# Optimization experiments

Measured on AMD Instinct MI355X. Metric: run time of the kernel, lower is better.

Reference implementation:

```python
import jax, jax.numpy as jnp
import numpy as np
from functools import partial

VOCAB = 32000
HID = 512
B, T = 16, 256


def setup_inputs() -> dict:
    key = jax.random.key(0)
    ks = jax.random.split(key, 14)
    s = 1.0 / np.sqrt(HID)
    u = lambda k, shape: jax.random.uniform(k, shape, jnp.float32, -s, s)
    inp = {
        "input_s": jax.random.randint(ks[0], (B, T), 0, VOCAB),
        "output_s": jax.random.randint(ks[1], (B, T), 0, VOCAB),
        "emb": jax.random.normal(ks[2], (VOCAB, HID), jnp.float32),
        "Wf": u(ks[3], (HID, 2 * HID)), "bf": u(ks[4], (HID,)),
        "Wi": u(ks[5], (HID, 2 * HID)), "bi": u(ks[6], (HID,)),
        "Wc": u(ks[7], (HID, 2 * HID)), "bc": u(ks[8], (HID,)),
        "Wo": u(ks[9], (HID, 2 * HID)), "bo": u(ks[10], (HID,)),
        "fcW": u(ks[11], (VOCAB, HID)), "fcb": u(ks[12], (VOCAB,)),
    }
    return inp


def reference(input_s, output_s, emb, Wf, bf, Wi, bi, Wc, bc, Wo, bo, fcW, fcb):
    bsz, width = input_s.shape
    x = emb[input_s]                      # [B, T, H]
    xs = jnp.swapaxes(x, 0, 1)            # [T, B, H] for scan
    h0 = jnp.zeros((bsz, HID), x.dtype)
    c0 = jnp.zeros((bsz, HID), x.dtype)

    def step(carry, xt):
        h, c = carry
        z = jnp.concatenate([h, xt], axis=1)       # [B, 2H], order (h, x) as in source
        f = jax.nn.sigmoid(z @ Wf.T + bf)
        i = jax.nn.sigmoid(z @ Wi.T + bi)
        cb = jnp.tanh(z @ Wc.T + bc)
        c = c * f + i * cb
        o = z @ Wo.T + bo                           # NOTE: no sigmoid (faithful to source)
        h = o * jnp.tanh(c)
        return (h, c), h

    _, hs = jax.lax.scan(step, (h0, c0), xs)        # hs: [T, B, H]
    hs = jnp.swapaxes(hs, 0, 1)                     # [B, T, H]
    logits = jnp.einsum("bth,vh->btv", hs, fcW) + fcb   # [B, T, V]
    logp = jax.nn.log_softmax(logits, axis=-1)
    nll = -jnp.take_along_axis(logp, output_s[..., None], axis=-1)[..., 0]
    loss = jnp.mean(nll)
    return logits, loss
```

## Files before the change

kernel.cpp:

```cpp
#include <hip/hip_runtime.h>

typedef unsigned short u16;
typedef __attribute__((ext_vector_type(8))) short bf16x8;
typedef __attribute__((ext_vector_type(4))) float f32x4;
typedef __attribute__((ext_vector_type(2))) float f32x2;
typedef __attribute__((ext_vector_type(4))) unsigned u32x4;

#define T_LEN 256
#define HID   512
#define VOCABN 32000
#define SCAN_WGS 16
#define FC_WORKERS 480
#define N_TILES 8000

__device__ __forceinline__ u16 f2bf(float f) {
  union { float f; unsigned u; } v; v.f = f;
  return (u16)((v.u + 0x7fffu + ((v.u >> 16) & 1u)) >> 16);
}
__device__ __forceinline__ float fast_tanh(float x) {
  return 1.f - 2.f / (__expf(2.f * x) + 1.f);
}

typedef __attribute__((address_space(1))) void as1v;
typedef __attribute__((address_space(3))) void as3v;
__device__ __forceinline__ void gload_lds16(const u16* g, u16* l) {
  __builtin_amdgcn_global_load_lds((as1v*)g, (as3v*)l, 16, 0, 0);
}

__global__ __launch_bounds__(256) void k_gather(const int* __restrict__ idx,
                                                const float* __restrict__ emb,
                                                u16* __restrict__ X) {
  int row0 = blockIdx.x * 8;
  for (int i = threadIdx.x; i < 8 * 128; i += 256) {
    int r = i >> 7, cb = i & 127;
    int row = row0 + r;
    int e = idx[row];
    float4 v = *(const float4*)&emb[(long)e * HID + cb * 4];
    ushort4 o; o.x = f2bf(v.x); o.y = f2bf(v.y); o.z = f2bf(v.z); o.w = f2bf(v.w);
    *(ushort4*)&X[(long)row * HID + cb * 4] = o;
  }
}

__global__ __launch_bounds__(256) void k_wconv(const float* __restrict__ Wf, const float* __restrict__ Wi,
                                               const float* __restrict__ Wc, const float* __restrict__ Wo,
                                               const float* __restrict__ bfv, const float* __restrict__ biv,
                                               const float* __restrict__ bcv, const float* __restrict__ bov,
                                               u16* __restrict__ Wh, u16* __restrict__ Wx,
                                               float* __restrict__ bias4) {
  int i = blockIdx.x * 256 + threadIdx.x;
  int r = i >> 7, kb = i & 127;
  int gate = r >> 9, j = r & 511;
  const float* W = gate == 0 ? Wf : gate == 1 ? Wi : gate == 2 ? Wc : Wo;
  float4 vh = *(const float4*)&W[(long)j * 1024 + kb * 4];
  float4 vx = *(const float4*)&W[(long)j * 1024 + 512 + kb * 4];
  ushort4 oh; oh.x = f2bf(vh.x); oh.y = f2bf(vh.y); oh.z = f2bf(vh.z); oh.w = f2bf(vh.w);
  ushort4 ox; ox.x = f2bf(vx.x); ox.y = f2bf(vx.y); ox.z = f2bf(vx.z); ox.w = f2bf(vx.w);
  *(ushort4*)&Wh[(long)r * 512 + kb * 4] = oh;
  *(ushort4*)&Wx[(long)r * 512 + kb * 4] = ox;
  if (kb == 0) {
    const float* bsrc = gate == 0 ? bfv : gate == 1 ? biv : gate == 2 ? bcv : bov;
    bias4[r] = bsrc[j];
  }
}

__global__ __launch_bounds__(256) void k_fcconv(const float* __restrict__ Wsrc, u16* __restrict__ Wdst) {
  long c = (long)blockIdx.x * 256 + threadIdx.x;
  float4 v = *(const float4*)&Wsrc[c * 4];
  ushort4 o; o.x = f2bf(v.x); o.y = f2bf(v.y); o.z = f2bf(v.z); o.w = f2bf(v.w);
  *(ushort4*)&Wdst[c * 4] = o;
}

__global__ __launch_bounds__(256) void k_gemm(const u16* __restrict__ A, const u16* __restrict__ B,
                                              const float* __restrict__ bias, float* __restrict__ C,
                                              int N) {
  __shared__ __align__(16) u16 As[128 * 32];
  __shared__ __align__(16) u16 Bs[128 * 32];
  const int K = 512;
  int tid = threadIdx.x, wave = tid >> 6, lane = tid & 63;
  int nbx = gridDim.x, nby = gridDim.y;
  int id = blockIdx.y * nbx + blockIdx.x;
  int nwg = nbx * nby, q = nwg >> 3;
  int swz = (id & 7) * q + (id >> 3);
  int bm = swz % nby, bn = swz / nby;
  int wr = wave >> 1, wc = wave & 1;
  f32x4 acc[4][4] = {};
  const u16* ga = A + (long)(bm * 128 + (tid >> 2)) * K + (tid & 3) * 8;
  const u16* gb = B + (long)(bn * 128 + (tid >> 2)) * K + (tid & 3) * 8;
  u16* lA = &As[wave * 512];
  u16* lB = &Bs[wave * 512];
  for (int kk = 0; kk < K; kk += 32) {
    gload_lds16(ga + kk, lA);
    gload_lds16(ga + 64 * K + kk, lA + 2048);
    gload_lds16(gb + kk, lB);
    gload_lds16(gb + 64 * K + kk, lB + 2048);
    __syncthreads();
    bf16x8 af[4], bfr[4];
    int arow = wr * 64 + (lane & 15);
    int brow = wc * 64 + (lane & 15);
    int kcol = (lane >> 4) * 8;
#pragma unroll
    for (int m = 0; m < 4; m++) af[m] = *(const bf16x8*)&As[(arow + m * 16) * 32 + kcol];
#pragma unroll
    for (int n = 0; n < 4; n++) bfr[n] = *(const bf16x8*)&Bs[(brow + n * 16) * 32 + kcol];
#pragma unroll
    for (int m = 0; m < 4; m++)
#pragma unroll
      for (int n = 0; n < 4; n++)
        acc[m][n] = __builtin_amdgcn_mfma_f32_16x16x32_bf16(af[m], bfr[n], acc[m][n], 0, 0, 0);
    __syncthreads();
  }
  int c0 = bn * 128 + wc * 64 + (lane & 15);
  int r0 = bm * 128 + wr * 64 + (lane >> 4) * 4;
#pragma unroll
  for (int n = 0; n < 4; n++) {
    float bv = bias[c0 + n * 16];
#pragma unroll
    for (int m = 0; m < 4; m++) {
      f32x4 v = acc[m][n];
#pragma unroll
      for (int rr = 0; rr < 4; rr++)
        C[(long)(r0 + m * 16 + rr) * N + (c0 + n * 16)] = v[rr] + bv;
    }
  }
}

__global__ __launch_bounds__(256, 2) void k_fused(
    const u16* __restrict__ Wh, const float* __restrict__ xw,
    u16* __restrict__ hs, unsigned* __restrict__ vf,
    const u16* __restrict__ fcWb, const float* __restrict__ fcb,
    float* __restrict__ C, float* __restrict__ part) {
  __shared__ __align__(16) char smraw[33408];
  int tid = threadIdx.x, wave = tid >> 6, lane = tid & 63;

  if (blockIdx.x < SCAN_WGS) {
    float* gates = (float*)smraw;
    u16*   Ash   = (u16*)(smraw + 17024);
    int g = blockIdx.x;
    int l4 = lane & 15, hi = lane >> 4;
    bf16x8 wreg[2][16];
#pragma unroll
    for (int n = 0; n < 2; n++) {
      int c = wave * 32 + n * 16 + l4;
      int grow = ((c >> 5) << 9) + (g << 5) + (c & 31);
      const u16* base = Wh + ((long)grow << 9) + (hi << 3);
#pragma unroll
      for (int kt = 0; kt < 16; kt++) wreg[n][kt] = *(const bf16x8*)(base + (kt << 5));
    }
    __builtin_amdgcn_s_setprio(1);

    float cs0 = 0.f, cs1 = 0.f;
    int u0 = (tid & 15) * 2, b = tid >> 4;
    const float* xwt = xw + ((long)b << 8) * 2048 + (g << 5) + u0;
    unsigned* vfp = vf + g * 32;

    for (int t = 0; t < T_LEN; t++) {
      f32x2 xv[4];
#pragma unroll
      for (int gt = 0; gt < 4; gt++) xv[gt] = *(const f32x2*)(xwt + (long)t * 2048 + (gt << 9));

      f32x4 acc[2] = {};
      if (t > 0) {
        if (wave == 0) {
          const u16* hrow = hs + (((long)(t - 1) * 16 + l4) << 9) + (hi << 3);
          bf16x8 af[16];
          for (;;) {
#pragma unroll
            for (int kt = 0; kt < 16; kt++)
              asm volatile("global_load_dwordx4 %0, %1, off sc0 sc1"
                           : "=v"(af[kt]) : "v"(hrow + (kt << 5)) : "memory");
            asm volatile("s_waitcnt vmcnt(0)" ::: "memory");
            __builtin_amdgcn_sched_barrier(0);
            unsigned mx = 0;
#pragma unroll
            for (int kt = 0; kt < 16; kt++) {
              u32x4 d = __builtin_bit_cast(u32x4, af[kt]);
              unsigned m0 = d.x > d.y ? d.x : d.y;
              unsigned m1 = d.z > d.w ? d.z : d.w;
              unsigned m2 = m0 > m1 ? m0 : m1;
              mx = mx > m2 ? mx : m2;
            }
            if (__all(mx != 0xFFFFFFFFu)) break;
            __builtin_amdgcn_s_sleep(2);
          }
#pragma unroll
          for (int kt = 0; kt < 16; kt++)
            *(bf16x8*)&Ash[(kt << 9) + (lane << 3)] = af[kt];
          if (lane == 0) {
            unsigned tv = (unsigned)t;
            asm volatile("global_store_dword %0, %1, off sc0 sc1" :: "v"(vfp), "v"(tv) : "memory");
          }
        }
        __syncthreads();
#pragma unroll
        for (int kt = 0; kt < 16; kt++) {
          bf16x8 afr = *(const bf16x8*)&Ash[(kt << 9) + (lane << 3)];
          acc[0] = __builtin_amdgcn_mfma_f32_16x16x32_bf16(afr, wreg[0][kt], acc[0], 0, 0, 0);
          acc[1] = __builtin_amdgcn_mfma_f32_16x16x32_bf16(afr, wreg[1][kt], acc[1], 0, 0, 0);
        }
      }
      int par = t & 1;
#pragma unroll
      for (int n = 0; n < 2; n++) {
        int c = wave * 32 + n * 16 + l4;
#pragma unroll
        for (int rr = 0; rr < 4; rr++) gates[(par * 16 + hi * 4 + rr) * 133 + c] = acc[n][rr];
      }
      __syncthreads();
      float p0[4], p1[4];
#pragma unroll
      for (int gt = 0; gt < 4; gt++) {
        p0[gt] = gates[(par * 16 + b) * 133 + (gt << 5) + u0]     + xv[gt].x;
        p1[gt] = gates[(par * 16 + b) * 133 + (gt << 5) + u0 + 1] + xv[gt].y;
      }
      float f0 = 1.f / (1.f + __expf(-p0[0]));
      float i0 = 1.f / (1.f + __expf(-p0[1]));
      cs0 = cs0 * f0 + i0 * fast_tanh(p0[2]);
      float h0 = p0[3] * fast_tanh(cs0);
      float f1 = 1.f / (1.f + __expf(-p1[0]));
      float i1 = 1.f / (1.f + __expf(-p1[1]));
      cs1 = cs1 * f1 + i1 * fast_tanh(p1[2]);
      float h1 = p1[3] * fast_tanh(cs1);

      unsigned hv = (unsigned)f2bf(h0) | ((unsigned)f2bf(h1) << 16);
      unsigned* hp = (unsigned*)(hs + (((long)t * 16 + b) << 9) + (g << 5) + u0);
      asm volatile("global_store_dword %0, %1, off sc0 sc1" :: "v"(hp), "v"(hv) : "memory");
    }
    if (wave == 0) {
      const u16* hrow = hs + (((long)255 * 16 + l4) << 9) + (hi << 3);
      for (;;) {
        bf16x8 af[16];
#pragma unroll
        for (int kt = 0; kt < 16; kt++)
          asm volatile("global_load_dwordx4 %0, %1, off sc0 sc1"
                       : "=v"(af[kt]) : "v"(hrow + (kt << 5)) : "memory");
        asm volatile("s_waitcnt vmcnt(0)" ::: "memory");
        __builtin_amdgcn_sched_barrier(0);
        unsigned mx = 0;
#pragma unroll
        for (int kt = 0; kt < 16; kt++) {
          u32x4 d = __builtin_bit_cast(u32x4, af[kt]);
          unsigned m0 = d.x > d.y ? d.x : d.y;
          unsigned m1 = d.z > d.w ? d.z : d.w;
          unsigned m2 = m0 > m1 ? m0 : m1;
          mx = mx > m2 ? mx : m2;
        }
        if (__all(mx != 0xFFFFFFFFu)) break;
        __builtin_amdgcn_s_sleep(2);
      }
      if (lane == 0) {
        unsigned fin = 256u;
        asm volatile("global_store_dword %0, %1, off sc0 sc1" :: "v"(vfp), "v"(fin) : "memory");
      }
    }
  } else {
    u16* As = (u16*)smraw;
    u16* Bs = (u16*)(smraw + 8192);
    const int K = 512;
    int wid = blockIdx.x - SCAN_WGS;
    int polled = -1;
    for (int tile = wid; tile < N_TILES; tile += FC_WORKERS) {
      int bm = tile / 250, bn = tile - bm * 250;
      if (bm > polled) {
        if (wave == 0) {
          const unsigned* fl = vf + (lane & 15) * 32;
          unsigned need = (unsigned)(bm * 8 + 8);
          for (;;) {
            unsigned v;
            asm volatile("global_load_dword %0, %1, off sc0 sc1\n\ts_waitcnt vmcnt(0)"
                         : "=v"(v) : "v"(fl) : "memory");
            if (__all((lane & 48) ? 1 : (v >= need))) break;
            __builtin_amdgcn_s_sleep(32);
          }
        }
        __syncthreads();
        polled = bm;
      }
      int wr = wave >> 1, wc = wave & 1;
      f32x4 acc[4][4] = {};
      const u16* ga = hs + (long)(bm * 128 + (tid >> 2)) * K + (tid & 3) * 8;
      const u16* gb = fcWb + (long)(bn * 128 + (tid >> 2)) * K + (tid & 3) * 8;
      u16* lB = &Bs[wave * 512];
      for (int kk = 0; kk < K; kk += 32) {
        gload_lds16(gb + kk, lB);
        gload_lds16(gb + 64 * K + kk, lB + 2048);
        bf16x8 a0, a1;
        asm volatile("global_load_dwordx4 %0, %1, off sc0 sc1" : "=v"(a0) : "v"(ga + kk));
        asm volatile("global_load_dwordx4 %0, %1, off sc0 sc1" : "=v"(a1) : "v"(ga + 64 * K + kk));
        asm volatile("s_waitcnt vmcnt(0)" ::: "memory");
        *(bf16x8*)&As[tid * 8] = a0;
        *(bf16x8*)&As[tid * 8 + 2048] = a1;
        __syncthreads();
        bf16x8 af[4], bfr[4];
        int arow = wr * 64 + (lane & 15);
        int brow = wc * 64 + (lane & 15);
        int kcol = (lane >> 4) * 8;
#pragma unroll
        for (int m = 0; m < 4; m++) af[m] = *(const bf16x8*)&As[(arow + m * 16) * 32 + kcol];
#pragma unroll
        for (int n = 0; n < 4; n++) bfr[n] = *(const bf16x8*)&Bs[(brow + n * 16) * 32 + kcol];
#pragma unroll
        for (int m = 0; m < 4; m++)
#pragma unroll
          for (int n = 0; n < 4; n++)
            acc[m][n] = __builtin_amdgcn_mfma_f32_16x16x32_bf16(af[m], bfr[n], acc[m][n], 0, 0, 0);
        __syncthreads();
      }
      int c0 = bn * 128 + wc * 64 + (lane & 15);
      float bv[4];
#pragma unroll
      for (int n = 0; n < 4; n++) bv[n] = fcb[c0 + n * 16];
#pragma unroll
      for (int m = 0; m < 4; m++) {
#pragma unroll
        for (int rr = 0; rr < 4; rr++) {
          int p = bm * 128 + wr * 64 + m * 16 + (lane >> 4) * 4 + rr;
          int row = (p & 15) * 256 + (p >> 4);
          float v0 = acc[m][0][rr] + bv[0];
          float v1 = acc[m][1][rr] + bv[1];
          float v2 = acc[m][2][rr] + bv[2];
          float v3 = acc[m][3][rr] + bv[3];
          float* Cr = C + (long)row * VOCABN + c0;
          __builtin_nontemporal_store(v0, &Cr[0]);
          __builtin_nontemporal_store(v1, &Cr[16]);
          __builtin_nontemporal_store(v2, &Cr[32]);
          __builtin_nontemporal_store(v3, &Cr[48]);
          float mx = fmaxf(fmaxf(v0, v1), fmaxf(v2, v3));
          float ss = __expf(v0 - mx) + __expf(v1 - mx) + __expf(v2 - mx) + __expf(v3 - mx);
#pragma unroll
          for (int d = 1; d < 16; d <<= 1) {
            float om = __shfl_xor(mx, d, 64);
            float os = __shfl_xor(ss, d, 64);
            float nm = fmaxf(mx, om);
            ss = ss * __expf(mx - nm) + os * __expf(om - nm);
            mx = nm;
          }
          if ((lane & 15) == 0) {
            f32x2 pr; pr.x = mx; pr.y = ss;
            __builtin_nontemporal_store(pr, (f32x2*)&part[((long)row * 500 + bn * 2 + wc) * 2]);
          }
        }
      }
    }
  }
}

__global__ __launch_bounds__(256) void k_nllred(const float* __restrict__ part,
                                                const float* __restrict__ logits,
                                                const int* __restrict__ tgt,
                                                float* __restrict__ nll) {
  int row = blockIdx.x * 4 + (threadIdx.x >> 6);
  int lane = threadIdx.x & 63;
  const float* P = part + (long)row * 1000;
  float m = -1e30f, s = 0.f;
  for (int p = lane; p < 500; p += 64) {
    float2 v = *(const float2*)&P[p * 2];
    float nm = fmaxf(m, v.x);
    s = s * __expf(m - nm) + v.y * __expf(v.x - nm);
    m = nm;
  }
#pragma unroll
  for (int d = 1; d < 64; d <<= 1) {
    float om = __shfl_xor(m, d, 64);
    float os = __shfl_xor(s, d, 64);
    float nm = fmaxf(m, om);
    s = s * __expf(m - nm) + os * __expf(om - nm);
    m = nm;
  }
  if (lane == 0)
    nll[row] = (m + __logf(s)) - logits[(long)row * VOCABN + tgt[row]];
}

__global__ __launch_bounds__(256) void k_loss(const float* __restrict__ nll, float* __restrict__ out) {
  __shared__ float sm[256];
  float acc = 0.f;
  for (int i = threadIdx.x; i < 4096; i += 256) acc += nll[i];
  sm[threadIdx.x] = acc;
  __syncthreads();
  for (int off = 128; off > 0; off >>= 1) {
    if (threadIdx.x < off) sm[threadIdx.x] += sm[threadIdx.x + off];
    __syncthreads();
  }
  if (threadIdx.x == 0) out[0] = sm[0] * (1.f / 4096.f);
}

extern "C" void kernel_launch(void* const* d_in, const int* in_sizes, int n_in,
                              void* d_out, int out_size, void* d_ws, size_t ws_size,
                              hipStream_t stream) {
  const int*   input_s  = (const int*)d_in[0];
  const int*   output_s = (const int*)d_in[1];
  const float* emb = (const float*)d_in[2];
  const float* Wf  = (const float*)d_in[3];
  const float* bfv = (const float*)d_in[4];
  const float* Wi  = (const float*)d_in[5];
  const float* biv = (const float*)d_in[6];
  const float* Wc  = (const float*)d_in[7];
  const float* bcv = (const float*)d_in[8];
  const float* Wo  = (const float*)d_in[9];
  const float* bov = (const float*)d_in[10];
  const float* fcW = (const float*)d_in[11];
  const float* fcb = (const float*)d_in[12];
  float* out = (float*)d_out;

  char* ws = (char*)d_ws;
  u16*      fcWb  = (u16*)(ws + 0);
  u16*      Wx    = (u16*)(ws + 32768000);
  u16*      Wh    = (u16*)(ws + 34865152);
  u16*      X     = (u16*)(ws + 36962304);
  float*    bias4 = (float*)(ws + 41156608);
  unsigned* vf    = (unsigned*)(ws + 41164800);
  float*    nll   = (float*)(ws + 41181312);
  u16*      hs    = (u16*)(ws + 41197696);
  float*    xw    = (float*)(ws + 45392000);
  float*    part  = (float*)(ws + 78946432);

  hipMemsetAsync(vf, 0, 2048, stream);
  hipMemsetAsync(hs, 0xFF, 4194304, stream);
  k_gather<<<512, 256, 0, stream>>>(input_s, emb, X);
  k_wconv<<<1024, 256, 0, stream>>>(Wf, Wi, Wc, Wo, bfv, biv, bcv, bov, Wh, Wx, bias4);
  k_fcconv<<<16000, 256, 0, stream>>>(fcW, fcWb);
  dim3 g1(16, 32);
  k_gemm<<<g1, 256, 0, stream>>>(X, Wx, bias4, xw, 2048);
  k_fused<<<SCAN_WGS + FC_WORKERS, 256, 0, stream>>>(Wh, xw, hs, vf, fcWb, fcb, out, part);
  k_nllred<<<1024, 256, 0, stream>>>(part, out, output_s, nll);
  k_loss<<<1, 256, 0, stream>>>(nll, out + 131072000L);
}
```

Baseline: 823.8 us.

## Compute LSTM gate nonlinearities in-register via lane shuffles, removing per-step LDS barrier

Remaps the recurrent weight columns so each wave's MFMA output holds all four gates for the same hidden units. Gate values are then exchanged across lanes with xor shuffles instead of being written to shared memory, which removes one __syncthreads per timestep. The h-tile staging buffer is double-buffered by timestep parity so only one barrier per step is still needed. The spin-wait now polls without sleeping for the first rounds and uses a shorter sleep afterwards. In exchange, the xw loads become scattered scalar loads, and only a quarter of the lanes issue the h stores.

```diff
diff --git a/kernel.cpp b/kernel.cpp
--- a/kernel.cpp
+++ b/kernel.cpp
@@ -129,40 +129,43 @@
     u16* __restrict__ hs, unsigned* __restrict__ vf,
     const u16* __restrict__ fcWb, const float* __restrict__ fcb,
     float* __restrict__ C, float* __restrict__ part) {
-  __shared__ __align__(16) char smraw[33408];
+  __shared__ __align__(16) char smraw[32768];
   int tid = threadIdx.x, wave = tid >> 6, lane = tid & 63;
 
   if (blockIdx.x < SCAN_WGS) {
-    float* gates = (float*)smraw;
-    u16*   Ash   = (u16*)(smraw + 17024);
+    u16* Ash = (u16*)smraw;
     int g = blockIdx.x;
-    int l4 = lane & 15, hi = lane >> 4;
+    int l4 = lane & 15, hi = lane >> 4, uu = l4 & 7;
     bf16x8 wreg[2][16];
 #pragma unroll
     for (int n = 0; n < 2; n++) {
-      int c = wave * 32 + n * 16 + l4;
-      int grow = ((c >> 5) << 9) + (g << 5) + (c & 31);
+      int gate = n * 2 + (l4 >> 3);
+      int grow = (gate << 9) + (g << 5) + (wave << 3) + uu;
       const u16* base = Wh + ((long)grow << 9) + (hi << 3);
 #pragma unroll
       for (int kt = 0; kt < 16; kt++) wreg[n][kt] = *(const bf16x8*)(base + (kt << 5));
     }
     __builtin_amdgcn_s_setprio(1);
 
-    float cs0 = 0.f, cs1 = 0.f;
-    int u0 = (tid & 15) * 2, b = tid >> 4;
-    const float* xwt = xw + ((long)b << 8) * 2048 + (g << 5) + u0;
+    float cs[4] = {0.f, 0.f, 0.f, 0.f};
+    int U = (g << 5) + (wave << 3) + uu;
+    const float* xb = xw + (long)(hi * 4) * 524288 + U;
     unsigned* vfp = vf + g * 32;
 
     for (int t = 0; t < T_LEN; t++) {
-      f32x2 xv[4];
-#pragma unroll
-      for (int gt = 0; gt < 4; gt++) xv[gt] = *(const f32x2*)(xwt + (long)t * 2048 + (gt << 9));
+      float xv[4][4];
+#pragma unroll
+      for (int rr = 0; rr < 4; rr++)
+#pragma unroll
+        for (int gate = 0; gate < 4; gate++)
+          xv[gate][rr] = xb[(long)rr * 524288 + (long)t * 2048 + (gate << 9)];
 
       f32x4 acc[2] = {};
       if (t > 0) {
         if (wave == 0) {
           const u16* hrow = hs + (((long)(t - 1) * 16 + l4) << 9) + (hi << 3);
           bf16x8 af[16];
+          int round = 0;
           for (;;) {
 #pragma unroll
             for (int kt = 0; kt < 16; kt++)
@@ -180,50 +183,51 @@
               mx = mx > m2 ? mx : m2;
             }
             if (__all(mx != 0xFFFFFFFFu)) break;
-            __builtin_amdgcn_s_sleep(2);
+            if (++round > 2) __builtin_amdgcn_s_sleep(1);
           }
+          u16* ad = &Ash[((t & 1) << 13)];
 #pragma unroll
           for (int kt = 0; kt < 16; kt++)
-            *(bf16x8*)&Ash[(kt << 9) + (lane << 3)] = af[kt];
+            *(bf16x8*)&ad[(kt << 9) + (lane << 3)] = af[kt];
           if (lane == 0) {
             unsigned tv = (unsigned)t;
             asm volatile("global_store_dword %0, %1, off sc0 sc1" :: "v"(vfp), "v"(tv) : "memory");
           }
         }
         __syncthreads();
+        const u16* ab = &Ash[((t & 1) << 13)];
 #pragma unroll
         for (int kt = 0; kt < 16; kt++) {
-          bf16x8 afr = *(const bf16x8*)&Ash[(kt << 9) + (lane << 3)];
+          bf16x8 afr = *(const bf16x8*)&ab[(kt << 9) + (lane << 3)];
           acc[0] = __builtin_amdgcn_mfma_f32_16x16x32_bf16(afr, wreg[0][kt], acc[0], 0, 0, 0);
           acc[1] = __builtin_amdgcn_mfma_f32_16x16x32_bf16(afr, wreg[1][kt], acc[1], 0, 0, 0);
         }
       }
-      int par = t & 1;
-#pragma unroll
-      for (int n = 0; n < 2; n++) {
-        int c = wave * 32 + n * 16 + l4;
-#pragma unroll
-        for (int rr = 0; rr < 4; rr++) gates[(par * 16 + hi * 4 + rr) * 133 + c] = acc[n][rr];
-      }
-      __syncthreads();
-      float p0[4], p1[4];
-#pragma unroll
-      for (int gt = 0; gt < 4; gt++) {
-        p0[gt] = gates[(par * 16 + b) * 133 + (gt << 5) + u0]     + xv[gt].x;
-        p1[gt] = gates[(par * 16 + b) * 133 + (gt << 5) + u0 + 1] + xv[gt].y;
-      }
-      float f0 = 1.f / (1.f + __expf(-p0[0]));
-      float i0 = 1.f / (1.f + __expf(-p0[1]));
-      cs0 = cs0 * f0 + i0 * fast_tanh(p0[2]);
-      float h0 = p0[3] * fast_tanh(cs0);
-      float f1 = 1.f / (1.f + __expf(-p1[0]));
-      float i1 = 1.f / (1.f + __expf(-p1[1]));
-      cs1 = cs1 * f1 + i1 * fast_tanh(p1[2]);
-      float h1 = p1[3] * fast_tanh(cs1);
-
-      unsigned hv = (unsigned)f2bf(h0) | ((unsigned)f2bf(h1) << 16);
-      unsigned* hp = (unsigned*)(hs + (((long)t * 16 + b) << 9) + (g << 5) + u0);
-      asm volatile("global_store_dword %0, %1, off sc0 sc1" :: "v"(hp), "v"(hv) : "memory");
+      bool lo = (l4 < 8);
+      float hval[4];
+#pragma unroll
+      for (int rr = 0; rr < 4; rr++) {
+        float a0 = acc[0][rr], a1 = acc[1][rr];
+        float b0 = __shfl_xor(a0, 8, 64);
+        float b1 = __shfl_xor(a1, 8, 64);
+        float fpre = (lo ? a0 : b0) + xv[0][rr];
+        float ipre = (lo ? b0 : a0) + xv[1][rr];
+        float cpre = (lo ? a1 : b1) + xv[2][rr];
+        float opre = (lo ? b1 : a1) + xv[3][rr];
+        float fg = 1.f / (1.f + __expf(-fpre));
+        float ig = 1.f / (1.f + __expf(-ipre));
+        cs[rr] = cs[rr] * fg + ig * fast_tanh(cpre);
+        hval[rr] = opre * fast_tanh(cs[rr]);
+      }
+#pragma unroll
+      for (int rr = 0; rr < 4; rr++) {
+        float hn = __shfl_xor(hval[rr], 1, 64);
+        if (lo && !(uu & 1)) {
+          unsigned hv = (unsigned)f2bf(hval[rr]) | ((unsigned)f2bf(hn) << 16);
+          unsigned* hp = (unsigned*)(hs + (((long)t * 16 + hi * 4 + rr) << 9) + U);
+          asm volatile("global_store_dword %0, %1, off sc0 sc1" :: "v"(hp), "v"(hv) : "memory");
+        }
+      }
     }
     if (wave == 0) {
       const u16* hrow = hs + (((long)255 * 16 + l4) << 9) + (hi << 3);
```

Result: slower. 997.2 us (+21.0%).

## Fuse fcW bf16 conversion into fused kernel's FC workers to overlap with scan

Applied to the files above, without the earlier changes.

Removes the separate fcW float-to-bf16 conversion kernel and has the FC worker blocks of the fused kernel do the conversion while the scan blocks run the recurrence. A global atomic counter and a spin barrier make sure every block has finished converting before any block starts the FC GEMM tiles. This hides the conversion's memory traffic behind the serial scan and removes one launch. The cost is that all FC workers must be co-resident for the barrier, and the stores use cache-bypass flags.

```diff
diff --git a/kernel.cpp b/kernel.cpp
--- a/kernel.cpp
+++ b/kernel.cpp
@@ -5,6 +5,7 @@
 typedef __attribute__((ext_vector_type(4))) float f32x4;
 typedef __attribute__((ext_vector_type(2))) float f32x2;
 typedef __attribute__((ext_vector_type(4))) unsigned u32x4;
+typedef __attribute__((ext_vector_type(2))) unsigned u32x2;
 
 #define T_LEN 256
 #define HID   512
@@ -61,13 +62,6 @@
     const float* bsrc = gate == 0 ? bfv : gate == 1 ? biv : gate == 2 ? bcv : bov;
     bias4[r] = bsrc[j];
   }
-}
-
-__global__ __launch_bounds__(256) void k_fcconv(const float* __restrict__ Wsrc, u16* __restrict__ Wdst) {
-  long c = (long)blockIdx.x * 256 + threadIdx.x;
-  float4 v = *(const float4*)&Wsrc[c * 4];
-  ushort4 o; o.x = f2bf(v.x); o.y = f2bf(v.y); o.z = f2bf(v.z); o.w = f2bf(v.w);
-  *(ushort4*)&Wdst[c * 4] = o;
 }
 
 __global__ __launch_bounds__(256) void k_gemm(const u16* __restrict__ A, const u16* __restrict__ B,
@@ -127,7 +121,8 @@
 __global__ __launch_bounds__(256, 2) void k_fused(
     const u16* __restrict__ Wh, const float* __restrict__ xw,
     u16* __restrict__ hs, unsigned* __restrict__ vf,
-    const u16* __restrict__ fcWb, const float* __restrict__ fcb,
+    const float* __restrict__ fcWsrc, u16* __restrict__ fcWb,
+    const float* __restrict__ fcb, unsigned* __restrict__ fcdone,
     float* __restrict__ C, float* __restrict__ part) {
   __shared__ __align__(16) char smraw[33408];
   int tid = threadIdx.x, wave = tid >> 6, lane = tid & 63;
@@ -257,6 +252,32 @@
     u16* Bs = (u16*)(smraw + 8192);
     const int K = 512;
     int wid = blockIdx.x - SCAN_WGS;
+
+    {
+      const float4* src = (const float4*)fcWsrc;
+      for (long c = (long)wid * 256 + tid; c < 4096000L; c += 480L * 256) {
+        float4 v = src[c];
+        unsigned lo = (unsigned)f2bf(v.x) | ((unsigned)f2bf(v.y) << 16);
+        unsigned hi2 = (unsigned)f2bf(v.z) | ((unsigned)f2bf(v.w) << 16);
+        u32x2 pk; pk.x = lo; pk.y = hi2;
+        asm volatile("global_store_dwordx2 %0, %1, off sc0 sc1"
+                     :: "v"(&fcWb[c * 4]), "v"(pk) : "memory");
+      }
+      asm volatile("s_waitcnt vmcnt(0)" ::: "memory");
+      __syncthreads();
+      if (tid == 0) atomicAdd(fcdone, 1u);
+      if (tid == 0) {
+        for (;;) {
+          unsigned v;
+          asm volatile("global_load_dword %0, %1, off sc0 sc1\n\ts_waitcnt vmcnt(0)"
+                       : "=v"(v) : "v"(fcdone) : "memory");
+          if (v >= (unsigned)FC_WORKERS) break;
+          __builtin_amdgcn_s_sleep(16);
+        }
+      }
+      __syncthreads();
+    }
+
     int polled = -1;
     for (int tile = wid; tile < N_TILES; tile += FC_WORKERS) {
       int bm = tile / 250, bn = tile - bm * 250;
@@ -408,19 +429,19 @@
   u16*      X     = (u16*)(ws + 36962304);
   float*    bias4 = (float*)(ws + 41156608);
   unsigned* vf    = (unsigned*)(ws + 41164800);
+  unsigned* fcdone= (unsigned*)(ws + 41166848);
   float*    nll   = (float*)(ws + 41181312);
   u16*      hs    = (u16*)(ws + 41197696);
   float*    xw    = (float*)(ws + 45392000);
   float*    part  = (float*)(ws + 78946432);
 
-  hipMemsetAsync(vf, 0, 2048, stream);
+  hipMemsetAsync(vf, 0, 2052, stream);
   hipMemsetAsync(hs, 0xFF, 4194304, stream);
   k_gather<<<512, 256, 0, stream>>>(input_s, emb, X);
   k_wconv<<<1024, 256, 0, stream>>>(Wf, Wi, Wc, Wo, bfv, biv, bcv, bov, Wh, Wx, bias4);
-  k_fcconv<<<16000, 256, 0, stream>>>(fcW, fcWb);
   dim3 g1(16, 32);
   k_gemm<<<g1, 256, 0, stream>>>(X, Wx, bias4, xw, 2048);
-  k_fused<<<SCAN_WGS + FC_WORKERS, 256, 0, stream>>>(Wh, xw, hs, vf, fcWb, fcb, out, part);
+  k_fused<<<SCAN_WGS + FC_WORKERS, 256, 0, stream>>>(Wh, xw, hs, vf, fcW, fcWb, fcb, fcdone, out, part);
   k_nllred<<<1024, 256, 0, stream>>>(part, out, output_s, nll);
   k_loss<<<1, 256, 0, stream>>>(nll, out + 131072000L);
 }
```

Result: no change. 827.4 us (+0.4%).
